# Optimization experiments

Measured on AMD Instinct MI355X. Metric: run time of the kernel, lower is better.

Reference implementation:

```python
import jax, jax.numpy as jnp
import numpy as np

B, M, K, F_IN, H = 64, 1024, 16, 4, 64  # B graphs of M nodes each, k=16 neighbors


def _knn_idx(h):
    # h: [B, M, H] -> indices of K nearest neighbors (excluding self): [B, M, K]
    sq = jnp.sum(h * h, axis=-1)                                   # [B, M]
    d = sq[:, :, None] + sq[:, None, :] - 2.0 * jnp.einsum('bmf,bnf->bmn', h, h)
    d = jnp.where(jnp.eye(M, dtype=bool)[None], jnp.float32(jnp.inf), d)
    _, idx = jax.lax.top_k(-d, K)                                  # smallest distances
    return idx


def _edge_conv(h, w1, b1, w2, b2):
    # Dynamic-graph EdgeConv with max aggregation (PyG default):
    # msg = MLP(concat[x_i, x_j - x_i]); out_i = max_j msg
    idx = _knn_idx(h)                                              # [B, M, K]
    x_j = jax.vmap(lambda hb, ib: hb[ib])(h, idx)                  # [B, M, K, H]
    x_i = jnp.broadcast_to(h[:, :, None, :], x_j.shape)
    msg = jnp.concatenate([x_i, x_j - x_i], axis=-1)               # [B, M, K, 2H]
    msg = jax.nn.relu(msg @ w1 + b1) @ w2 + b2                     # [B, M, K, H]
    return jnp.max(msg, axis=2)                                    # [B, M, H]


def setup_inputs() -> dict:
    key = jax.random.key(0)
    ks = jax.random.split(key, 20)

    def lin(k, fi, fo):
        return jax.random.normal(k, (fi, fo), jnp.float32) / np.sqrt(fi)

    inp = {
        'x': jax.random.normal(ks[0], (B * M, F_IN), jnp.float32),
        'batch': jnp.repeat(jnp.arange(B, dtype=jnp.int64), M),
        # encoder: Linear(4,32) ReLU Linear(32,64) ReLU
        'enc_w1': lin(ks[1], F_IN, 32), 'enc_b1': jnp.zeros((32,), jnp.float32),
        'enc_w2': lin(ks[2], 32, H),    'enc_b2': jnp.zeros((H,), jnp.float32),
        # EdgeConv MLPs: Linear(128,64) ReLU Linear(64,64)
        'ec1_w1': lin(ks[3], 2 * H, H), 'ec1_b1': jnp.zeros((H,), jnp.float32),
        'ec1_w2': lin(ks[4], H, H),     'ec1_b2': jnp.zeros((H,), jnp.float32),
        'ec2_w1': lin(ks[5], 2 * H, H), 'ec2_b1': jnp.zeros((H,), jnp.float32),
        'ec2_w2': lin(ks[6], H, H),     'ec2_b2': jnp.zeros((H,), jnp.float32),
        # output MLP: Linear(64,32) ReLU Linear(32,1)
        'out_w1': lin(ks[7], H, 32),    'out_b1': jnp.zeros((32,), jnp.float32),
        'out_w2': lin(ks[8], 32, 1),    'out_b2': jnp.zeros((1,), jnp.float32),
    }
    return inp


def reference(x, batch, enc_w1, enc_b1, enc_w2, enc_b2,
              ec1_w1, ec1_b1, ec1_w2, ec1_b2,
              ec2_w1, ec2_b1, ec2_w2, ec2_b2,
              out_w1, out_b1, out_w2, out_b2):
    # batch is repeat(arange(B), M): equal-size graphs -> reshape into [B, M, .]
    h = jax.nn.relu(jax.nn.relu(x @ enc_w1 + enc_b1) @ enc_w2 + enc_b2)  # [N, 64]
    h = h.reshape(B, M, H)
    h = _edge_conv(h, ec1_w1, ec1_b1, ec1_w2, ec1_b2)
    h = _edge_conv(h, ec2_w1, ec2_b1, ec2_w2, ec2_b2)
    g = jnp.mean(h, axis=1)                                        # global_mean_pool -> [B, 64]
    out = jax.nn.relu(g @ out_w1 + out_b1) @ out_w2 + out_b2       # [B, 1]
    return out.reshape(-1)                                         # [B]
```

## Files before the change

### kernel.cpp

```cpp
#include <hip/hip_runtime.h>
#include <math.h>

#define B_ 64
#define M_ 1024
#define H_ 64
#define N_ (B_*M_)

typedef _Float16 half8 __attribute__((ext_vector_type(8)));
typedef float  floatx4 __attribute__((ext_vector_type(4)));

#define MFMA16(a,b,c) __builtin_amdgcn_mfma_f32_16x16x32_f16(a,b,c,0,0,0)
#define MED3(a,b,c)   __builtin_amdgcn_fmed3f(a,b,c)

__global__ __launch_bounds__(256) void enc_kernel(
    const float* __restrict__ x,
    const float* __restrict__ w1,
    const float* __restrict__ b1,
    const float* __restrict__ w2,
    const float* __restrict__ b2,
    float* __restrict__ h,
    _Float16* __restrict__ hhi,
    _Float16* __restrict__ hlo,
    float* __restrict__ sq)
{
    __shared__ float sw1[4*32];
    __shared__ float sb1[32];
    __shared__ float sw2[32*64];
    __shared__ float sb2[64];
    int t = threadIdx.x;
    for (int i = t; i < 128; i += 256) sw1[i] = w1[i];
    if (t < 32) sb1[t] = b1[t];
    for (int i = t; i < 2048; i += 256) sw2[i] = w2[i];
    if (t < 64) sb2[t] = b2[t];
    __syncthreads();
    int n = blockIdx.x * 256 + t;
    float4 xv = *(const float4*)(x + (size_t)n*4);
    float hid[32];
    #pragma unroll
    for (int o = 0; o < 32; ++o) {
        float a = sb1[o] + xv.x*sw1[0*32+o] + xv.y*sw1[1*32+o]
                        + xv.z*sw1[2*32+o] + xv.w*sw1[3*32+o];
        hid[o] = fmaxf(a, 0.f);
    }
    float* hout = h + (size_t)n*64;
    float sqa = 0.f;
    #pragma unroll 4
    for (int oc = 0; oc < 16; ++oc) {
        float4 acc = make_float4(sb2[oc*4+0], sb2[oc*4+1], sb2[oc*4+2], sb2[oc*4+3]);
        #pragma unroll
        for (int f = 0; f < 32; ++f) {
            float4 w = *(const float4*)(sw2 + f*64 + oc*4);
            float hv = hid[f];
            acc.x += hv*w.x; acc.y += hv*w.y; acc.z += hv*w.z; acc.w += hv*w.w;
        }
        acc.x = fmaxf(acc.x,0.f); acc.y = fmaxf(acc.y,0.f);
        acc.z = fmaxf(acc.z,0.f); acc.w = fmaxf(acc.w,0.f);
        *(float4*)(hout + oc*4) = acc;
        sqa += acc.x*acc.x + acc.y*acc.y + acc.z*acc.z + acc.w*acc.w;
        union { _Float16 f[4]; uint2 u; } Hh, Hl;
        Hh.f[0]=(_Float16)acc.x; Hh.f[1]=(_Float16)acc.y;
        Hh.f[2]=(_Float16)acc.z; Hh.f[3]=(_Float16)acc.w;
        Hl.f[0]=(_Float16)(acc.x-(float)Hh.f[0]); Hl.f[1]=(_Float16)(acc.y-(float)Hh.f[1]);
        Hl.f[2]=(_Float16)(acc.z-(float)Hh.f[2]); Hl.f[3]=(_Float16)(acc.w-(float)Hh.f[3]);
        *(uint2*)(hhi + (size_t)n*64 + oc*4) = Hh.u;
        *(uint2*)(hlo + (size_t)n*64 + oc*4) = Hl.u;
    }
    sq[n] = sqa;
}

__global__ __launch_bounds__(256) void convert_kernel(
    const float* __restrict__ h,
    _Float16* __restrict__ hhi, _Float16* __restrict__ hlo,
    float* __restrict__ sq)
{
    int t = threadIdx.x, lane = t & 63, w = t >> 6;
    int base = blockIdx.x * 64 + w * 16;
    for (int it = 0; it < 16; ++it) {
        int i = base + it;
        float v = h[(size_t)i*64 + lane];
        _Float16 hi = (_Float16)v;
        _Float16 lo = (_Float16)(v - (float)hi);
        hhi[(size_t)i*64 + lane] = hi;
        hlo[(size_t)i*64 + lane] = lo;
        float s = v*v;
        #pragma unroll
        for (int off = 1; off < 64; off <<= 1) s += __shfl_xor(s, off, 64);
        if (lane == 0) sq[i] = s;
    }
}

__global__ __launch_bounds__(256) void gemmA_kernel(
    const float* __restrict__ h,
    const float* __restrict__ w1,
    float* __restrict__ A)
{
    __shared__ float sw[64*64];
    int t = threadIdx.x;
    for (int idx = t; idx < 4096; idx += 256) sw[idx] = w1[4096 + idx];
    __syncthreads();
    int n = blockIdx.x * 256 + t;
    float4 hv[16];
    const float* src = h + (size_t)n*64;
    #pragma unroll
    for (int c = 0; c < 16; ++c) hv[c] = *(const float4*)(src + c*4);
    float* dst = A + (size_t)n*64;
    #pragma unroll 2
    for (int oc = 0; oc < 16; ++oc) {
        float4 acc = make_float4(0.f,0.f,0.f,0.f);
        #pragma unroll
        for (int f = 0; f < 64; ++f) {
            float xv = ((const float*)hv)[f];
            float4 w = *(const float4*)(sw + f*64 + oc*4);
            acc.x += xv*w.x; acc.y += xv*w.y; acc.z += xv*w.z; acc.w += xv*w.w;
        }
        *(float4*)(dst + oc*4) = acc;
    }
}

__global__ __launch_bounds__(256) void knn_kernel(
    const _Float16* __restrict__ hhi,
    const _Float16* __restrict__ hlo,
    const float* __restrict__ sqg,
    unsigned short* __restrict__ knn)
{
    __shared__ float D[4][64*33];
    __shared__ float sqS[1024];
    int t = threadIdx.x, lane = t & 63, w = t >> 6;
    int bi = blockIdx.x;
    int g  = (bi & 7) | ((bi >> 7) << 3);
    int qt = (bi >> 3) & 15;
    const _Float16* hhig = hhi + (size_t)g*M_*64;
    const _Float16* hlog = hlo + (size_t)g*M_*64;
    const float*    sqb  = sqg + (size_t)g*M_;
    ((float4*)sqS)[t] = ((const float4*)sqb)[t];

    int m16  = lane & 15;
    int koct = (lane >> 4) * 8;
    half8 Ahi[4][2], Alo[4][2];
    #pragma unroll
    for (int rb = 0; rb < 4; ++rb) {
        const _Float16* ph = hhig + (size_t)(qt*64 + rb*16 + m16)*64;
        const _Float16* pl = hlog + (size_t)(qt*64 + rb*16 + m16)*64;
        Ahi[rb][0] = *(const half8*)(ph + koct);
        Ahi[rb][1] = *(const half8*)(ph + 32 + koct);
        Alo[rb][0] = *(const half8*)(pl + koct);
        Alo[rb][1] = *(const half8*)(pl + 32 + koct);
    }
    float* Dw   = D[w];
    int    crow = (lane >> 4) * 4;
    float  bd[16];
    #pragma unroll
    for (int k = 0; k < 16; ++k) bd[k] = INFINITY;
    int cand0 = w*256;
    __syncthreads();
    float c1 = 1.f + sqS[qt*64 + lane];
    int selfc_all = qt*64 + lane;

    #pragma unroll
    for (int cc = 0; cc < 8; ++cc) {
        int cbase = cand0 + cc*32;
        half8 Bhi[2][2], Blo[2][2];
        #pragma unroll
        for (int cb = 0; cb < 2; ++cb) {
            const _Float16* ph = hhig + (size_t)(cbase + cb*16 + m16)*64;
            const _Float16* pl = hlog + (size_t)(cbase + cb*16 + m16)*64;
            Bhi[cb][0] = *(const half8*)(ph + koct);
            Bhi[cb][1] = *(const half8*)(ph + 32 + koct);
            Blo[cb][0] = *(const half8*)(pl + koct);
            Blo[cb][1] = *(const half8*)(pl + 32 + koct);
        }
        #pragma unroll
        for (int rb = 0; rb < 4; ++rb) {
            #pragma unroll
            for (int cb = 0; cb < 2; ++cb) {
                floatx4 acc = {0.f, 0.f, 0.f, 0.f};
                acc = MFMA16(Ahi[rb][0], Bhi[cb][0], acc);
                acc = MFMA16(Ahi[rb][1], Bhi[cb][1], acc);
                acc = MFMA16(Ahi[rb][0], Blo[cb][0], acc);
                acc = MFMA16(Ahi[rb][1], Blo[cb][1], acc);
                acc = MFMA16(Alo[rb][0], Bhi[cb][0], acc);
                acc = MFMA16(Alo[rb][1], Bhi[cb][1], acc);
                #pragma unroll
                for (int r = 0; r < 4; ++r)
                    Dw[(rb*16 + crow + r)*33 + cb*16 + m16] = acc[r];
            }
        }
        const float* drow = Dw + lane*33;
        int selfc = selfc_all - cbase;
        #pragma unroll
        for (int c8 = 0; c8 < 4; ++c8) {
            float sv[8], qv[8];
            #pragma unroll
            for (int j = 0; j < 8; ++j) {
                sv[j] = drow[c8*8 + j];
                qv[j] = sqS[cbase + c8*8 + j];
            }
            #pragma unroll
            for (int j = 0; j < 8; ++j) {
                int c = c8*8 + j;
                float s  = fmaf(-2.f, sv[j], qv[j]);
                float t2 = c1 + s;
                unsigned kb = (__float_as_uint(t2) & 0xFFFFFC00u)
                            | (unsigned)(cbase + c);
                float fk = __uint_as_float(kb);
                if (c == selfc) fk = INFINITY;
                float nb0 = fminf(bd[0], fk);
                #pragma unroll
                for (int k = 15; k >= 1; --k) bd[k] = MED3(fk, bd[k-1], bd[k]);
                bd[0] = nb0;
            }
        }
    }

    __syncthreads();
    float* md = &D[0][0];
    #pragma unroll
    for (int k = 0; k < 16; ++k) md[lane*65 + w*16 + k] = bd[k];
    __syncthreads();
    if (w == 0) {
        float b2[16];
        #pragma unroll
        for (int k = 0; k < 16; ++k) b2[k] = INFINITY;
        const float* mrow = md + lane*65;
        #pragma unroll
        for (int c8 = 0; c8 < 8; ++c8) {
            float sv[8];
            #pragma unroll
            for (int j = 0; j < 8; ++j) sv[j] = mrow[c8*8 + j];
            #pragma unroll
            for (int j = 0; j < 8; ++j) {
                float s = sv[j];
                float nb0 = fminf(b2[0], s);
                #pragma unroll
                for (int k = 15; k >= 1; --k) b2[k] = MED3(s, b2[k-1], b2[k]);
                b2[0] = nb0;
            }
        }
        union { unsigned short us[16]; uint4 v4[2]; } o;
        #pragma unroll
        for (int k = 0; k < 16; ++k)
            o.us[k] = (unsigned short)(__float_as_uint(b2[k]) & 1023u);
        size_t gq = (size_t)g*M_ + qt*64 + lane;
        uint4* dst = (uint4*)(knn + gq*16);
        dst[0] = o.v4[0];
        dst[1] = o.v4[1];
    }
}

__global__ __launch_bounds__(256) void edge_kernel(
    const float* __restrict__ h,
    const float* __restrict__ A,
    const unsigned short* __restrict__ knn,
    const float* __restrict__ w1,
    const float* __restrict__ b1,
    const float* __restrict__ w2,
    const float* __restrict__ b2,
    float* __restrict__ hout)
{
    __shared__ __align__(16) _Float16 wdf[16*64*8];
    __shared__ __align__(16) _Float16 w2f[16*64*8];
    float* CsB = (float*)w2f;
    int t = threadIdx.x;
    for (int u = t; u < 512; u += 256) {
        int ulane = u & 63, nt = u >> 7, ks = (u >> 6) & 1;
        int n = nt*16 + (ulane & 15);
        int kbase = ks*32 + ((ulane >> 4) * 8);
        int fh = (((nt*2+ks)*2+0)*64 + ulane)*8;
        int fl = (((nt*2+ks)*2+1)*64 + ulane)*8;
        #pragma unroll
        for (int j = 0; j < 8; ++j) {
            int k = kbase + j;
            float vd = w1[k*64+n] - w1[4096 + k*64+n];
            _Float16 dh = (_Float16)vd;
            wdf[fh+j] = dh;
            wdf[fl+j] = (_Float16)(vd - (float)dh);
            float v2 = w2[k*64+n];
            _Float16 h2 = (_Float16)v2;
            w2f[fh+j] = h2;
            w2f[fl+j] = (_Float16)(v2 - (float)h2);
        }
    }
    __syncthreads();
    int lane = t & 63, wid = t >> 6;
    int m16 = lane & 15, gid = lane >> 4;
    int koct = gid*8, crow = gid*4;
    int bi = blockIdx.x;
    int g  = (bi & 7) | ((bi >> 7) << 3);
    int qt = (bi >> 3) & 15;
    int i0 = g*M_ + qt*64 + wid*16;
    const float* Ab = A + (size_t)g*M_*H_;

    half8 W2r[4][2][2];
    #pragma unroll
    for (int nt = 0; nt < 4; ++nt)
        #pragma unroll
        for (int ks = 0; ks < 2; ++ks)
            #pragma unroll
            for (int p = 0; p < 2; ++p)
                W2r[nt][ks][p] = *(const half8*)&w2f[(((nt*2+ks)*2+p)*64+lane)*8];

    float b1v[4];
    #pragma unroll
    for (int nt = 0; nt < 4; ++nt) b1v[nt] = b1[nt*16+m16];
    float b2v = b2[gid*16+m16];
    __syncthreads();

    half8 Hh[2], Hl[2];
    #pragma unroll
    for (int ks = 0; ks < 2; ++ks) {
        const float* hp = h + (size_t)(i0+m16)*64 + ks*32 + koct;
        float4 v0 = *(const float4*)hp;
        float4 v1 = *(const float4*)(hp+4);
        float va[8] = {v0.x,v0.y,v0.z,v0.w,v1.x,v1.y,v1.z,v1.w};
        #pragma unroll
        for (int j = 0; j < 8; ++j) {
            _Float16 hi = (_Float16)va[j];
            Hh[ks][j] = hi;
            Hl[ks][j] = (_Float16)(va[j]-(float)hi);
        }
    }
    #pragma unroll
    for (int nt = 0; nt < 4; ++nt) {
        floatx4 acc = {b1v[nt], b1v[nt], b1v[nt], b1v[nt]};
        #pragma unroll
        for (int ks = 0; ks < 2; ++ks) {
            half8 wh = *(const half8*)&wdf[(((nt*2+ks)*2+0)*64+lane)*8];
            half8 wl = *(const half8*)&wdf[(((nt*2+ks)*2+1)*64+lane)*8];
            acc = MFMA16(Hh[ks], wh, acc);
            acc = MFMA16(Hh[ks], wl, acc);
            acc = MFMA16(Hl[ks], wh, acc);
        }
        #pragma unroll
        for (int r = 0; r < 4; ++r)
            CsB[((wid*16) + crow + r)*64 + nt*16 + m16] = acc[r];
    }
    __syncthreads();

    const unsigned short* knb = knn + (size_t)i0*16;
    #pragma unroll 2
    for (int nn = 0; nn < 16; ++nn) {
        int j = knb[nn*16 + m16];
        const float* Ap = Ab + (size_t)j*64;
        half8 Mh[2], Ml[2];
        #pragma unroll
        for (int ks = 0; ks < 2; ++ks) {
            float4 a0 = *(const float4*)(Ap + ks*32 + koct);
            float4 a1 = *(const float4*)(Ap + ks*32 + koct + 4);
            const float* cp = &CsB[(wid*16 + nn)*64 + ks*32 + koct];
            float4 c0 = *(const float4*)cp;
            float4 c1 = *(const float4*)(cp+4);
            float mv[8] = {
                fmaxf(a0.x+c0.x,0.f), fmaxf(a0.y+c0.y,0.f),
                fmaxf(a0.z+c0.z,0.f), fmaxf(a0.w+c0.w,0.f),
                fmaxf(a1.x+c1.x,0.f), fmaxf(a1.y+c1.y,0.f),
                fmaxf(a1.z+c1.z,0.f), fmaxf(a1.w+c1.w,0.f)};
            #pragma unroll
            for (int jj = 0; jj < 8; ++jj) {
                _Float16 hi = (_Float16)mv[jj];
                Mh[ks][jj] = hi;
                Ml[ks][jj] = (_Float16)(mv[jj]-(float)hi);
            }
        }
        floatx4 acc[4];
        #pragma unroll
        for (int nt = 0; nt < 4; ++nt) {
            acc[nt] = (floatx4){0.f,0.f,0.f,0.f};
            #pragma unroll
            for (int ks = 0; ks < 2; ++ks) {
                acc[nt] = MFMA16(Mh[ks], W2r[nt][ks][0], acc[nt]);
                acc[nt] = MFMA16(Mh[ks], W2r[nt][ks][1], acc[nt]);
                acc[nt] = MFMA16(Ml[ks], W2r[nt][ks][0], acc[nt]);
            }
        }
        float om[4];
        #pragma unroll
        for (int nt = 0; nt < 4; ++nt) {
            float mr = fmaxf(fmaxf(acc[nt][0], acc[nt][1]),
                             fmaxf(acc[nt][2], acc[nt][3]));
            mr = fmaxf(mr, __shfl_xor(mr, 16, 64));
            mr = fmaxf(mr, __shfl_xor(mr, 32, 64));
            om[nt] = mr;
        }
        float val = (gid == 0) ? om[0] : (gid == 1) ? om[1]
                  : (gid == 2) ? om[2] : om[3];
        hout[(size_t)(i0+nn)*64 + gid*16 + m16] = val + b2v;
    }
}

__global__ __launch_bounds__(256) void pool_kernel(
    const float* __restrict__ h,
    const float* __restrict__ w1,
    const float* __restrict__ b1,
    const float* __restrict__ w2,
    const float* __restrict__ b2,
    float* __restrict__ out)
{
    __shared__ float part[4][64];
    __shared__ float g[64];
    __shared__ float hid[32];
    int t = threadIdx.x;
    int o = t & 63, p = t >> 6;
    int b = blockIdx.x;
    const float* hb = h + (size_t)b*M_*H_;
    float s = 0.f;
    for (int m = p; m < M_; m += 4) s += hb[(size_t)m*64 + o];
    part[p][o] = s;
    __syncthreads();
    if (t < 64) g[t] = (part[0][t] + part[1][t] + part[2][t] + part[3][t]) * (1.f/M_);
    __syncthreads();
    if (t < 32) {
        float a = b1[t];
        for (int f = 0; f < 64; ++f) a += g[f] * w1[f*32 + t];
        hid[t] = fmaxf(a, 0.f);
    }
    __syncthreads();
    if (t == 0) {
        float a = b2[0];
        for (int f = 0; f < 32; ++f) a += hid[f] * w2[f];
        out[b] = a;
    }
}

extern "C" void kernel_launch(void* const* d_in, const int* in_sizes, int n_in,
                              void* d_out, int out_size, void* d_ws, size_t ws_size,
                              hipStream_t stream)
{
    (void)in_sizes; (void)n_in; (void)out_size; (void)ws_size;
    const float* x      = (const float*)d_in[0];
    const float* enc_w1 = (const float*)d_in[2];
    const float* enc_b1 = (const float*)d_in[3];
    const float* enc_w2 = (const float*)d_in[4];
    const float* enc_b2 = (const float*)d_in[5];
    const float* ec1_w1 = (const float*)d_in[6];
    const float* ec1_b1 = (const float*)d_in[7];
    const float* ec1_w2 = (const float*)d_in[8];
    const float* ec1_b2 = (const float*)d_in[9];
    const float* ec2_w1 = (const float*)d_in[10];
    const float* ec2_b1 = (const float*)d_in[11];
    const float* ec2_w2 = (const float*)d_in[12];
    const float* ec2_b2 = (const float*)d_in[13];
    const float* out_w1 = (const float*)d_in[14];
    const float* out_b1 = (const float*)d_in[15];
    const float* out_w2 = (const float*)d_in[16];
    const float* out_b2 = (const float*)d_in[17];

    char* ws = (char*)d_ws;
    float*          h   = (float*)(ws);
    char*           r2  = ws + (size_t)N_*64*4;
    _Float16*       hhi = (_Float16*)r2;
    _Float16*       hlo = (_Float16*)(r2 + (size_t)N_*64*2);
    float*          A   = (float*)r2;
    unsigned short* idx = (unsigned short*)(ws + (size_t)N_*64*4*2);
    float*          sq  = (float*)(ws + (size_t)N_*64*4*2 + (size_t)N_*16*2);

    enc_kernel<<<N_/256, 256, 0, stream>>>(x, enc_w1, enc_b1, enc_w2, enc_b2,
                                           h, hhi, hlo, sq);
    knn_kernel <<<B_*16, 256, 0, stream>>>(hhi, hlo, sq, idx);
    gemmA_kernel<<<N_/256, 256, 0, stream>>>(h, ec1_w1, A);
    edge_kernel<<<N_/64, 256, 0, stream>>>(h, A, idx, ec1_w1, ec1_b1, ec1_w2, ec1_b2, h);
    convert_kernel<<<N_/64, 256, 0, stream>>>(h, hhi, hlo, sq);
    knn_kernel <<<B_*16, 256, 0, stream>>>(hhi, hlo, sq, idx);
    gemmA_kernel<<<N_/256, 256, 0, stream>>>(h, ec2_w1, A);
    edge_kernel<<<N_/64, 256, 0, stream>>>(h, A, idx, ec2_w1, ec2_b1, ec2_w2, ec2_b2, h);
    pool_kernel<<<B_, 256, 0, stream>>>(h, out_w1, out_b1, out_w2, out_b2, (float*)d_out);
}
```

Baseline: 420.7 us.

## Drop fp32 activations, fuse hi/lo split into edge epilogue, pipeline knn loads

The fp32 activation buffer is removed: the encoder and edge kernels write only the fp16 hi/lo pair and the squared norms, and later consumers (gemmA, edge, pool) rebuild values from hi+lo. This removes the separate convert kernel and the fp32 traffic it and the encoder caused. The knn kernel's candidate loop is also rewritten with double-buffered B loads, so the next tile's global loads are issued before the current tile is scanned. The cost is extra conversion ALU in the consumers and higher register pressure in knn.

```diff
diff --git a/kernel.cpp b/kernel.cpp
--- a/kernel.cpp
+++ b/kernel.cpp
@@ -18,7 +18,6 @@
     const float* __restrict__ b1,
     const float* __restrict__ w2,
     const float* __restrict__ b2,
-    float* __restrict__ h,
     _Float16* __restrict__ hhi,
     _Float16* __restrict__ hlo,
     float* __restrict__ sq)
@@ -42,7 +41,6 @@
                         + xv.z*sw1[2*32+o] + xv.w*sw1[3*32+o];
         hid[o] = fmaxf(a, 0.f);
     }
-    float* hout = h + (size_t)n*64;
     float sqa = 0.f;
     #pragma unroll 4
     for (int oc = 0; oc < 16; ++oc) {
@@ -55,7 +53,6 @@
         }
         acc.x = fmaxf(acc.x,0.f); acc.y = fmaxf(acc.y,0.f);
         acc.z = fmaxf(acc.z,0.f); acc.w = fmaxf(acc.w,0.f);
-        *(float4*)(hout + oc*4) = acc;
         sqa += acc.x*acc.x + acc.y*acc.y + acc.z*acc.z + acc.w*acc.w;
         union { _Float16 f[4]; uint2 u; } Hh, Hl;
         Hh.f[0]=(_Float16)acc.x; Hh.f[1]=(_Float16)acc.y;
@@ -68,29 +65,9 @@
     sq[n] = sqa;
 }
 
-__global__ __launch_bounds__(256) void convert_kernel(
-    const float* __restrict__ h,
-    _Float16* __restrict__ hhi, _Float16* __restrict__ hlo,
-    float* __restrict__ sq)
-{
-    int t = threadIdx.x, lane = t & 63, w = t >> 6;
-    int base = blockIdx.x * 64 + w * 16;
-    for (int it = 0; it < 16; ++it) {
-        int i = base + it;
-        float v = h[(size_t)i*64 + lane];
-        _Float16 hi = (_Float16)v;
-        _Float16 lo = (_Float16)(v - (float)hi);
-        hhi[(size_t)i*64 + lane] = hi;
-        hlo[(size_t)i*64 + lane] = lo;
-        float s = v*v;
-        #pragma unroll
-        for (int off = 1; off < 64; off <<= 1) s += __shfl_xor(s, off, 64);
-        if (lane == 0) sq[i] = s;
-    }
-}
-
 __global__ __launch_bounds__(256) void gemmA_kernel(
-    const float* __restrict__ h,
+    const _Float16* __restrict__ hhi,
+    const _Float16* __restrict__ hlo,
     const float* __restrict__ w1,
     float* __restrict__ A)
 {
@@ -99,21 +76,97 @@
     for (int idx = t; idx < 4096; idx += 256) sw[idx] = w1[4096 + idx];
     __syncthreads();
     int n = blockIdx.x * 256 + t;
-    float4 hv[16];
-    const float* src = h + (size_t)n*64;
-    #pragma unroll
-    for (int c = 0; c < 16; ++c) hv[c] = *(const float4*)(src + c*4);
+    float hv[64];
+    const _Float16* sh = hhi + (size_t)n*64;
+    const _Float16* sl = hlo + (size_t)n*64;
+    #pragma unroll
+    for (int c = 0; c < 8; ++c) {
+        half8 a = *(const half8*)(sh + c*8);
+        half8 b = *(const half8*)(sl + c*8);
+        #pragma unroll
+        for (int j = 0; j < 8; ++j) hv[c*8+j] = (float)a[j] + (float)b[j];
+    }
     float* dst = A + (size_t)n*64;
     #pragma unroll 2
     for (int oc = 0; oc < 16; ++oc) {
         float4 acc = make_float4(0.f,0.f,0.f,0.f);
         #pragma unroll
         for (int f = 0; f < 64; ++f) {
-            float xv = ((const float*)hv)[f];
+            float xv = hv[f];
             float4 w = *(const float4*)(sw + f*64 + oc*4);
             acc.x += xv*w.x; acc.y += xv*w.y; acc.z += xv*w.z; acc.w += xv*w.w;
         }
         *(float4*)(dst + oc*4) = acc;
+    }
+}
+
+__device__ __forceinline__ void knn_loadB(
+    half8 (&BH)[2][2], half8 (&BL)[2][2],
+    const _Float16* __restrict__ hhig, const _Float16* __restrict__ hlog,
+    int cb0, int m16, int koct)
+{
+    #pragma unroll
+    for (int cb = 0; cb < 2; ++cb) {
+        const _Float16* ph = hhig + (size_t)(cb0 + cb*16 + m16)*64;
+        const _Float16* pl = hlog + (size_t)(cb0 + cb*16 + m16)*64;
+        BH[cb][0] = *(const half8*)(ph + koct);
+        BH[cb][1] = *(const half8*)(ph + 32 + koct);
+        BL[cb][0] = *(const half8*)(pl + koct);
+        BL[cb][1] = *(const half8*)(pl + 32 + koct);
+    }
+}
+
+__device__ __forceinline__ void knn_mfma(
+    const half8 (&BH)[2][2], const half8 (&BL)[2][2],
+    const half8 (&Ahi)[4][2], const half8 (&Alo)[4][2],
+    float* __restrict__ Dw, int crow, int m16)
+{
+    #pragma unroll
+    for (int rb = 0; rb < 4; ++rb) {
+        #pragma unroll
+        for (int cb = 0; cb < 2; ++cb) {
+            floatx4 acc = {0.f, 0.f, 0.f, 0.f};
+            acc = MFMA16(Ahi[rb][0], BH[cb][0], acc);
+            acc = MFMA16(Ahi[rb][1], BH[cb][1], acc);
+            acc = MFMA16(Ahi[rb][0], BL[cb][0], acc);
+            acc = MFMA16(Ahi[rb][1], BL[cb][1], acc);
+            acc = MFMA16(Alo[rb][0], BH[cb][0], acc);
+            acc = MFMA16(Alo[rb][1], BH[cb][1], acc);
+            #pragma unroll
+            for (int r = 0; r < 4; ++r)
+                Dw[(rb*16 + crow + r)*33 + cb*16 + m16] = acc[r];
+        }
+    }
+}
+
+__device__ __forceinline__ void knn_scan(
+    const float* __restrict__ Dw, const float* __restrict__ sqS,
+    float (&bd)[16], int cbase, int selfc_all, int lane, float c1)
+{
+    const float* drow = Dw + lane*33;
+    int selfc = selfc_all - cbase;
+    #pragma unroll
+    for (int c8 = 0; c8 < 4; ++c8) {
+        float sv[8], qv[8];
+        #pragma unroll
+        for (int j = 0; j < 8; ++j) {
+            sv[j] = drow[c8*8 + j];
+            qv[j] = sqS[cbase + c8*8 + j];
+        }
+        #pragma unroll
+        for (int j = 0; j < 8; ++j) {
+            int c = c8*8 + j;
+            float s  = fmaf(-2.f, sv[j], qv[j]);
+            float t2 = c1 + s;
+            unsigned kb = (__float_as_uint(t2) & 0xFFFFFC00u)
+                        | (unsigned)(cbase + c);
+            float fk = __uint_as_float(kb);
+            if (c == selfc) fk = INFINITY;
+            float nb0 = fminf(bd[0], fk);
+            #pragma unroll
+            for (int k = 15; k >= 1; --k) bd[k] = MED3(fk, bd[k-1], bd[k]);
+            bd[0] = nb0;
+        }
     }
 }
 
@@ -156,61 +209,39 @@
     float c1 = 1.f + sqS[qt*64 + lane];
     int selfc_all = qt*64 + lane;
 
-    #pragma unroll
-    for (int cc = 0; cc < 8; ++cc) {
-        int cbase = cand0 + cc*32;
-        half8 Bhi[2][2], Blo[2][2];
-        #pragma unroll
-        for (int cb = 0; cb < 2; ++cb) {
-            const _Float16* ph = hhig + (size_t)(cbase + cb*16 + m16)*64;
-            const _Float16* pl = hlog + (size_t)(cbase + cb*16 + m16)*64;
-            Bhi[cb][0] = *(const half8*)(ph + koct);
-            Bhi[cb][1] = *(const half8*)(ph + 32 + koct);
-            Blo[cb][0] = *(const half8*)(pl + koct);
-            Blo[cb][1] = *(const half8*)(pl + 32 + koct);
-        }
-        #pragma unroll
-        for (int rb = 0; rb < 4; ++rb) {
-            #pragma unroll
-            for (int cb = 0; cb < 2; ++cb) {
-                floatx4 acc = {0.f, 0.f, 0.f, 0.f};
-                acc = MFMA16(Ahi[rb][0], Bhi[cb][0], acc);
-                acc = MFMA16(Ahi[rb][1], Bhi[cb][1], acc);
-                acc = MFMA16(Ahi[rb][0], Blo[cb][0], acc);
-                acc = MFMA16(Ahi[rb][1], Blo[cb][1], acc);
-                acc = MFMA16(Alo[rb][0], Bhi[cb][0], acc);
-                acc = MFMA16(Alo[rb][1], Bhi[cb][1], acc);
-                #pragma unroll
-                for (int r = 0; r < 4; ++r)
-                    Dw[(rb*16 + crow + r)*33 + cb*16 + m16] = acc[r];
-            }
-        }
-        const float* drow = Dw + lane*33;
-        int selfc = selfc_all - cbase;
-        #pragma unroll
-        for (int c8 = 0; c8 < 4; ++c8) {
-            float sv[8], qv[8];
-            #pragma unroll
-            for (int j = 0; j < 8; ++j) {
-                sv[j] = drow[c8*8 + j];
-                qv[j] = sqS[cbase + c8*8 + j];
-            }
-            #pragma unroll
-            for (int j = 0; j < 8; ++j) {
-                int c = c8*8 + j;
-                float s  = fmaf(-2.f, sv[j], qv[j]);
-                float t2 = c1 + s;
-                unsigned kb = (__float_as_uint(t2) & 0xFFFFFC00u)
-                            | (unsigned)(cbase + c);
-                float fk = __uint_as_float(kb);
-                if (c == selfc) fk = INFINITY;
-                float nb0 = fminf(bd[0], fk);
-                #pragma unroll
-                for (int k = 15; k >= 1; --k) bd[k] = MED3(fk, bd[k-1], bd[k]);
-                bd[0] = nb0;
-            }
-        }
-    }
+    half8 B0h[2][2], B0l[2][2], B1h[2][2], B1l[2][2];
+    knn_loadB(B0h, B0l, hhig, hlog, cand0 + 0*32, m16, koct);
+    knn_loadB(B1h, B1l, hhig, hlog, cand0 + 1*32, m16, koct);
+
+    knn_mfma(B0h, B0l, Ahi, Alo, Dw, crow, m16);
+    knn_loadB(B0h, B0l, hhig, hlog, cand0 + 2*32, m16, koct);
+    knn_scan(Dw, sqS, bd, cand0 + 0*32, selfc_all, lane, c1);
+
+    knn_mfma(B1h, B1l, Ahi, Alo, Dw, crow, m16);
+    knn_loadB(B1h, B1l, hhig, hlog, cand0 + 3*32, m16, koct);
+    knn_scan(Dw, sqS, bd, cand0 + 1*32, selfc_all, lane, c1);
+
+    knn_mfma(B0h, B0l, Ahi, Alo, Dw, crow, m16);
+    knn_loadB(B0h, B0l, hhig, hlog, cand0 + 4*32, m16, koct);
+    knn_scan(Dw, sqS, bd, cand0 + 2*32, selfc_all, lane, c1);
+
+    knn_mfma(B1h, B1l, Ahi, Alo, Dw, crow, m16);
+    knn_loadB(B1h, B1l, hhig, hlog, cand0 + 5*32, m16, koct);
+    knn_scan(Dw, sqS, bd, cand0 + 3*32, selfc_all, lane, c1);
+
+    knn_mfma(B0h, B0l, Ahi, Alo, Dw, crow, m16);
+    knn_loadB(B0h, B0l, hhig, hlog, cand0 + 6*32, m16, koct);
+    knn_scan(Dw, sqS, bd, cand0 + 4*32, selfc_all, lane, c1);
+
+    knn_mfma(B1h, B1l, Ahi, Alo, Dw, crow, m16);
+    knn_loadB(B1h, B1l, hhig, hlog, cand0 + 7*32, m16, koct);
+    knn_scan(Dw, sqS, bd, cand0 + 5*32, selfc_all, lane, c1);
+
+    knn_mfma(B0h, B0l, Ahi, Alo, Dw, crow, m16);
+    knn_scan(Dw, sqS, bd, cand0 + 6*32, selfc_all, lane, c1);
+
+    knn_mfma(B1h, B1l, Ahi, Alo, Dw, crow, m16);
+    knn_scan(Dw, sqS, bd, cand0 + 7*32, selfc_all, lane, c1);
 
     __syncthreads();
     float* md = &D[0][0];
@@ -248,14 +279,15 @@
 }
 
 __global__ __launch_bounds__(256) void edge_kernel(
-    const float* __restrict__ h,
+    _Float16* __restrict__ hhi,
+    _Float16* __restrict__ hlo,
     const float* __restrict__ A,
     const unsigned short* __restrict__ knn,
     const float* __restrict__ w1,
     const float* __restrict__ b1,
     const float* __restrict__ w2,
     const float* __restrict__ b2,
-    float* __restrict__ hout)
+    float* __restrict__ sqo)
 {
     __shared__ __align__(16) _Float16 wdf[16*64*8];
     __shared__ __align__(16) _Float16 w2f[16*64*8];
@@ -308,16 +340,8 @@
     half8 Hh[2], Hl[2];
     #pragma unroll
     for (int ks = 0; ks < 2; ++ks) {
-        const float* hp = h + (size_t)(i0+m16)*64 + ks*32 + koct;
-        float4 v0 = *(const float4*)hp;
-        float4 v1 = *(const float4*)(hp+4);
-        float va[8] = {v0.x,v0.y,v0.z,v0.w,v1.x,v1.y,v1.z,v1.w};
-        #pragma unroll
-        for (int j = 0; j < 8; ++j) {
-            _Float16 hi = (_Float16)va[j];
-            Hh[ks][j] = hi;
-            Hl[ks][j] = (_Float16)(va[j]-(float)hi);
-        }
+        Hh[ks] = *(const half8*)(hhi + (size_t)(i0+m16)*64 + ks*32 + koct);
+        Hl[ks] = *(const half8*)(hlo + (size_t)(i0+m16)*64 + ks*32 + koct);
     }
     #pragma unroll
     for (int nt = 0; nt < 4; ++nt) {
@@ -383,12 +407,21 @@
         }
         float val = (gid == 0) ? om[0] : (gid == 1) ? om[1]
                   : (gid == 2) ? om[2] : om[3];
-        hout[(size_t)(i0+nn)*64 + gid*16 + m16] = val + b2v;
+        float ov = val + b2v;
+        _Float16 oh = (_Float16)ov;
+        _Float16 ol = (_Float16)(ov - (float)oh);
+        hhi[(size_t)(i0+nn)*64 + lane] = oh;
+        hlo[(size_t)(i0+nn)*64 + lane] = ol;
+        float ss = ov*ov;
+        #pragma unroll
+        for (int off = 1; off < 64; off <<= 1) ss += __shfl_xor(ss, off, 64);
+        if (lane == 0) sqo[i0+nn] = ss;
     }
 }
 
 __global__ __launch_bounds__(256) void pool_kernel(
-    const float* __restrict__ h,
+    const _Float16* __restrict__ hhi,
+    const _Float16* __restrict__ hlo,
     const float* __restrict__ w1,
     const float* __restrict__ b1,
     const float* __restrict__ w2,
@@ -401,9 +434,11 @@
     int t = threadIdx.x;
     int o = t & 63, p = t >> 6;
     int b = blockIdx.x;
-    const float* hb = h + (size_t)b*M_*H_;
+    const _Float16* hb = hhi + (size_t)b*M_*H_;
+    const _Float16* lb = hlo + (size_t)b*M_*H_;
     float s = 0.f;
-    for (int m = p; m < M_; m += 4) s += hb[(size_t)m*64 + o];
+    for (int m = p; m < M_; m += 4)
+        s += (float)hb[(size_t)m*64 + o] + (float)lb[(size_t)m*64 + o];
     part[p][o] = s;
     __syncthreads();
     if (t < 64) g[t] = (part[0][t] + part[1][t] + part[2][t] + part[3][t]) * (1.f/M_);
@@ -445,22 +480,22 @@
     const float* out_b2 = (const float*)d_in[17];
 
     char* ws = (char*)d_ws;
-    float*          h   = (float*)(ws);
-    char*           r2  = ws + (size_t)N_*64*4;
-    _Float16*       hhi = (_Float16*)r2;
-    _Float16*       hlo = (_Float16*)(r2 + (size_t)N_*64*2);
-    float*          A   = (float*)r2;
-    unsigned short* idx = (unsigned short*)(ws + (size_t)N_*64*4*2);
-    float*          sq  = (float*)(ws + (size_t)N_*64*4*2 + (size_t)N_*16*2);
+    _Float16*       hhi = (_Float16*)(ws);
+    _Float16*       hlo = (_Float16*)(ws + (size_t)N_*64*2);
+    float*          A   = (float*)   (ws + (size_t)N_*64*4);
+    unsigned short* idx = (unsigned short*)(ws + (size_t)N_*64*8);
+    float*          sq  = (float*)   (ws + (size_t)N_*64*8 + (size_t)N_*16*2);
 
     enc_kernel<<<N_/256, 256, 0, stream>>>(x, enc_w1, enc_b1, enc_w2, enc_b2,
-                                           h, hhi, hlo, sq);
+                                           hhi, hlo, sq);
     knn_kernel <<<B_*16, 256, 0, stream>>>(hhi, hlo, sq, idx);
-    gemmA_kernel<<<N_/256, 256, 0, stream>>>(h, ec1_w1, A);
-    edge_kernel<<<N_/64, 256, 0, stream>>>(h, A, idx, ec1_w1, ec1_b1, ec1_w2, ec1_b2, h);
-    convert_kernel<<<N_/64, 256, 0, stream>>>(h, hhi, hlo, sq);
+    gemmA_kernel<<<N_/256, 256, 0, stream>>>(hhi, hlo, ec1_w1, A);
+    edge_kernel<<<N_/64, 256, 0, stream>>>(hhi, hlo, A, idx,
+                                           ec1_w1, ec1_b1, ec1_w2, ec1_b2, sq);
     knn_kernel <<<B_*16, 256, 0, stream>>>(hhi, hlo, sq, idx);
-    gemmA_kernel<<<N_/256, 256, 0, stream>>>(h, ec2_w1, A);
-    edge_kernel<<<N_/64, 256, 0, stream>>>(h, A, idx, ec2_w1, ec2_b1, ec2_w2, ec2_b2, h);
-    pool_kernel<<<B_, 256, 0, stream>>>(h, out_w1, out_b1, out_w2, out_b2, (float*)d_out);
-}
+    gemmA_kernel<<<N_/256, 256, 0, stream>>>(hhi, hlo, ec2_w1, A);
+    edge_kernel<<<N_/64, 256, 0, stream>>>(hhi, hlo, A, idx,
+                                           ec2_w1, ec2_b1, ec2_w2, ec2_b2, sq);
+    pool_kernel<<<B_, 256, 0, stream>>>(hhi, hlo, out_w1, out_b1, out_w2, out_b2,
+                                        (float*)d_out);
+}
```

Result: slower. 467.3 us (+11.1%).

## Halve kNN query tile per block and fold distance terms into MFMA accumulator

Applied to the files above, without the earlier changes.

The kNN kernel now handles 32 queries per block instead of 64, doubling the grid. Each query's candidate range per wave is split between two lanes, so all 64 lanes are busy on half-width top-16 insertion, and the final merge now combines 8 partial lists per query. The -2 scale is folded into the A fragments and the squared-norm terms are preloaded into the MFMA accumulator, which removes the per-candidate fma and the sqS reads in the selection loop. The trade-off is twice as many candidate fragment loads across blocks, a longer final merge serialized on 32 threads, and a small precision change from scaling the fp16 values by -2.

```diff
diff --git a/kernel.cpp b/kernel.cpp
--- a/kernel.cpp
+++ b/kernel.cpp
@@ -123,12 +123,12 @@
     const float* __restrict__ sqg,
     unsigned short* __restrict__ knn)
 {
-    __shared__ float D[4][64*33];
+    __shared__ float D[4][32*33];
     __shared__ float sqS[1024];
     int t = threadIdx.x, lane = t & 63, w = t >> 6;
     int bi = blockIdx.x;
-    int g  = (bi & 7) | ((bi >> 7) << 3);
-    int qt = (bi >> 3) & 15;
+    int g  = (bi & 7) | ((bi >> 8) << 3);
+    int qt = (bi >> 3) & 31;
     const _Float16* hhig = hhi + (size_t)g*M_*64;
     const _Float16* hlog = hlo + (size_t)g*M_*64;
     const float*    sqb  = sqg + (size_t)g*M_;
@@ -136,25 +136,42 @@
 
     int m16  = lane & 15;
     int koct = (lane >> 4) * 8;
-    half8 Ahi[4][2], Alo[4][2];
-    #pragma unroll
-    for (int rb = 0; rb < 4; ++rb) {
-        const _Float16* ph = hhig + (size_t)(qt*64 + rb*16 + m16)*64;
-        const _Float16* pl = hlog + (size_t)(qt*64 + rb*16 + m16)*64;
+    int crow = (lane >> 4) * 4;
+    half8 Ahi[2][2], Alo[2][2];
+    #pragma unroll
+    for (int rb = 0; rb < 2; ++rb) {
+        const _Float16* ph = hhig + (size_t)(qt*32 + rb*16 + m16)*64;
+        const _Float16* pl = hlog + (size_t)(qt*32 + rb*16 + m16)*64;
         Ahi[rb][0] = *(const half8*)(ph + koct);
         Ahi[rb][1] = *(const half8*)(ph + 32 + koct);
         Alo[rb][0] = *(const half8*)(pl + koct);
         Alo[rb][1] = *(const half8*)(pl + 32 + koct);
     }
-    float* Dw   = D[w];
-    int    crow = (lane >> 4) * 4;
-    float  bd[16];
+    #pragma unroll
+    for (int rb = 0; rb < 2; ++rb)
+        #pragma unroll
+        for (int p = 0; p < 2; ++p)
+            #pragma unroll
+            for (int j = 0; j < 8; ++j) {
+                Ahi[rb][p][j] = Ahi[rb][p][j] * (_Float16)-2.0f;
+                Alo[rb][p][j] = Alo[rb][p][j] * (_Float16)-2.0f;
+            }
+    __syncthreads();
+    float c1r[2][4];
+    #pragma unroll
+    for (int rb = 0; rb < 2; ++rb)
+        #pragma unroll
+        for (int r = 0; r < 4; ++r)
+            c1r[rb][r] = 1.f + sqS[qt*32 + rb*16 + crow + r];
+
+    float* Dw = D[w];
+    float bd[16];
     #pragma unroll
     for (int k = 0; k < 16; ++k) bd[k] = INFINITY;
     int cand0 = w*256;
-    __syncthreads();
-    float c1 = 1.f + sqS[qt*64 + lane];
-    int selfc_all = qt*64 + lane;
+    int qloc  = lane & 31;
+    int halfo = (lane >> 5) << 4;
+    int selfc_all = qt*32 + qloc;
 
     #pragma unroll
     for (int cc = 0; cc < 8; ++cc) {
@@ -170,10 +187,12 @@
             Blo[cb][1] = *(const half8*)(pl + 32 + koct);
         }
         #pragma unroll
-        for (int rb = 0; rb < 4; ++rb) {
+        for (int rb = 0; rb < 2; ++rb) {
             #pragma unroll
             for (int cb = 0; cb < 2; ++cb) {
-                floatx4 acc = {0.f, 0.f, 0.f, 0.f};
+                float sqj = sqS[cbase + cb*16 + m16];
+                floatx4 acc = {c1r[rb][0]+sqj, c1r[rb][1]+sqj,
+                               c1r[rb][2]+sqj, c1r[rb][3]+sqj};
                 acc = MFMA16(Ahi[rb][0], Bhi[cb][0], acc);
                 acc = MFMA16(Ahi[rb][1], Bhi[cb][1], acc);
                 acc = MFMA16(Ahi[rb][0], Blo[cb][0], acc);
@@ -185,25 +204,20 @@
                     Dw[(rb*16 + crow + r)*33 + cb*16 + m16] = acc[r];
             }
         }
-        const float* drow = Dw + lane*33;
-        int selfc = selfc_all - cbase;
-        #pragma unroll
-        for (int c8 = 0; c8 < 4; ++c8) {
-            float sv[8], qv[8];
+        const float* drow = Dw + qloc*33 + halfo;
+        int cb0 = cbase + halfo;
+        #pragma unroll
+        for (int c8 = 0; c8 < 2; ++c8) {
+            float sv[8];
+            #pragma unroll
+            for (int j = 0; j < 8; ++j) sv[j] = drow[c8*8 + j];
             #pragma unroll
             for (int j = 0; j < 8; ++j) {
-                sv[j] = drow[c8*8 + j];
-                qv[j] = sqS[cbase + c8*8 + j];
-            }
-            #pragma unroll
-            for (int j = 0; j < 8; ++j) {
-                int c = c8*8 + j;
-                float s  = fmaf(-2.f, sv[j], qv[j]);
-                float t2 = c1 + s;
-                unsigned kb = (__float_as_uint(t2) & 0xFFFFFC00u)
-                            | (unsigned)(cbase + c);
+                int cand = cb0 + c8*8 + j;
+                unsigned kb = (__float_as_uint(sv[j]) & 0xFFFFFC00u)
+                            | (unsigned)cand;
                 float fk = __uint_as_float(kb);
-                if (c == selfc) fk = INFINITY;
+                if (cand == selfc_all) fk = INFINITY;
                 float nb0 = fminf(bd[0], fk);
                 #pragma unroll
                 for (int k = 15; k >= 1; --k) bd[k] = MED3(fk, bd[k-1], bd[k]);
@@ -214,16 +228,17 @@
 
     __syncthreads();
     float* md = &D[0][0];
-    #pragma unroll
-    for (int k = 0; k < 16; ++k) md[lane*65 + w*16 + k] = bd[k];
-    __syncthreads();
-    if (w == 0) {
+    int slot = (w << 1) | (lane >> 5);
+    #pragma unroll
+    for (int k = 0; k < 16; ++k) md[qloc*130 + slot*16 + k] = bd[k];
+    __syncthreads();
+    if (t < 32) {
         float b2[16];
         #pragma unroll
         for (int k = 0; k < 16; ++k) b2[k] = INFINITY;
-        const float* mrow = md + lane*65;
-        #pragma unroll
-        for (int c8 = 0; c8 < 8; ++c8) {
+        const float* mrow = md + t*130;
+        #pragma unroll
+        for (int c8 = 0; c8 < 16; ++c8) {
             float sv[8];
             #pragma unroll
             for (int j = 0; j < 8; ++j) sv[j] = mrow[c8*8 + j];
@@ -240,7 +255,7 @@
         #pragma unroll
         for (int k = 0; k < 16; ++k)
             o.us[k] = (unsigned short)(__float_as_uint(b2[k]) & 1023u);
-        size_t gq = (size_t)g*M_ + qt*64 + lane;
+        size_t gq = (size_t)g*M_ + qt*32 + t;
         uint4* dst = (uint4*)(knn + gq*16);
         dst[0] = o.v4[0];
         dst[1] = o.v4[1];
@@ -455,11 +470,11 @@
 
     enc_kernel<<<N_/256, 256, 0, stream>>>(x, enc_w1, enc_b1, enc_w2, enc_b2,
                                            h, hhi, hlo, sq);
-    knn_kernel <<<B_*16, 256, 0, stream>>>(hhi, hlo, sq, idx);
+    knn_kernel <<<B_*32, 256, 0, stream>>>(hhi, hlo, sq, idx);
     gemmA_kernel<<<N_/256, 256, 0, stream>>>(h, ec1_w1, A);
     edge_kernel<<<N_/64, 256, 0, stream>>>(h, A, idx, ec1_w1, ec1_b1, ec1_w2, ec1_b2, h);
     convert_kernel<<<N_/64, 256, 0, stream>>>(h, hhi, hlo, sq);
-    knn_kernel <<<B_*16, 256, 0, stream>>>(hhi, hlo, sq, idx);
+    knn_kernel <<<B_*32, 256, 0, stream>>>(hhi, hlo, sq, idx);
     gemmA_kernel<<<N_/256, 256, 0, stream>>>(h, ec2_w1, A);
     edge_kernel<<<N_/64, 256, 0, stream>>>(h, A, idx, ec2_w1, ec2_b1, ec2_w2, ec2_b2, h);
     pool_kernel<<<B_, 256, 0, stream>>>(h, out_w1, out_b1, out_w2, out_b2, (float*)d_out);
```

Measured after the change: 448.9 us. +6.7%, slower.
